# Kernel optimization log

Measured on AMD Instinct MI355X. Metric: run time of the kernel, lower is better.

The kernel has to match this reference:

```python
import jax, jax.numpy as jnp
import numpy as np

B, TX, TY, D, H, DK, DFF, L, V = 64, 200, 100, 512, 8, 64, 2048, 4, 30


def _ln(x, g, b, eps=1e-5):
    m = x.mean(-1, keepdims=True)
    v = x.var(-1, keepdims=True)  # biased, matches torch LayerNorm
    return (x - m) * jax.lax.rsqrt(v + eps) * g + b


def _mha(k_in, v_in, q_in, qkv, pw, pb, pad_mask, causal):
    # qkv: [3, H, DK, D] (torch Linear layout [out, in]); scale uses C = d_model
    scale = float(q_in.shape[-1]) ** 0.5
    Q = jnp.einsum('btd,hkd->bhtk', q_in, qkv[0])
    K = jnp.einsum('bsd,hkd->bhsk', k_in, qkv[1])
    Vv = jnp.einsum('bsd,hvd->bhsv', v_in, qkv[2])
    W = jnp.einsum('bhtk,bhsk->bhts', Q, K) / scale  # [B,H,T,S]
    if causal:
        tril = jnp.tril(jnp.ones((q_in.shape[1], k_in.shape[1]), bool))
        W = jnp.where(tril, W, -jnp.inf)
    if pad_mask is not None:
        W = jnp.where(pad_mask[:, None] == 1, -jnp.inf, W)
    A = jax.nn.softmax(W, axis=-1)
    out = jnp.einsum('bhts,bhsv->bhtv', A, Vv)
    b_, h_, t_, dv = out.shape
    out = out.transpose(0, 2, 1, 3).reshape(b_, t_, h_ * dv)  # concat heads
    return out @ pw.T + pb


def _attn_block(k, v, q, qkv, pw, pb, g, b, pad_mask, causal):
    kn, vn, qn = _ln(k, g, b), _ln(v, g, b), _ln(q, g, b)
    # NOTE: residual from the NORMED query, as in the original code
    return qn + _mha(kn, vn, qn, qkv, pw, pb, pad_mask, causal)


def _ff_block(x, w1, b1, w2, b2, g, b):
    h = jax.nn.relu(_ln(x, g, b) @ w1.T + b1)
    return x + h @ w2.T + b2


def _forward(x, y, enc_qkv, enc_proj_w, enc_proj_b, enc_ln1_g, enc_ln1_b,
             enc_ff_w1, enc_ff_b1, enc_ff_w2, enc_ff_b2, enc_ln2_g, enc_ln2_b,
             dec_sa_qkv, dec_sa_proj_w, dec_sa_proj_b, dec_ln1_g, dec_ln1_b,
             dec_ca_qkv, dec_ca_proj_w, dec_ca_proj_b, dec_ln2_g, dec_ln2_b,
             dec_ff_w1, dec_ff_b1, dec_ff_w2, dec_ff_b2, dec_ln3_g, dec_ln3_b,
             ll_w, ll_b, x_mask, y_mask):
    enc = x
    for i in range(L):
        enc = _attn_block(enc, enc, enc, enc_qkv[i], enc_proj_w[i], enc_proj_b[i],
                          enc_ln1_g[i], enc_ln1_b[i], x_mask, False)
        enc = _ff_block(enc, enc_ff_w1[i], enc_ff_b1[i], enc_ff_w2[i], enc_ff_b2[i],
                        enc_ln2_g[i], enc_ln2_b[i])
    dec = y
    for i in range(L):
        dec = _attn_block(dec, dec, dec, dec_sa_qkv[i], dec_sa_proj_w[i], dec_sa_proj_b[i],
                          dec_ln1_g[i], dec_ln1_b[i], y_mask, True)
        dec = _attn_block(enc, enc, dec, dec_ca_qkv[i], dec_ca_proj_w[i], dec_ca_proj_b[i],
                          dec_ln2_g[i], dec_ln2_b[i], None, False)
        dec = _ff_block(dec, dec_ff_w1[i], dec_ff_b1[i], dec_ff_w2[i], dec_ff_b2[i],
                        dec_ln3_g[i], dec_ln3_b[i])
    return dec @ ll_w.T + ll_b


def setup_inputs() -> dict:
    key = jax.random.key(0)
    ks = iter(jax.random.split(key, 64))

    def nrm(shape, s=0.02):
        return jax.random.normal(next(ks), shape, jnp.float32) * s

    return dict(
        x=nrm((B, TX, D), 1.0), y=nrm((B, TY, D), 1.0),
        x_mask=jnp.zeros((B, TX, TX), jnp.int32),
        y_mask=jnp.zeros((B, TY, TY), jnp.int32),
        enc_qkv=nrm((L, 3, H, DK, D)), enc_proj_w=nrm((L, D, D)), enc_proj_b=jnp.zeros((L, D)),
        enc_ln1_g=jnp.ones((L, D)), enc_ln1_b=jnp.zeros((L, D)),
        enc_ff_w1=nrm((L, DFF, D)), enc_ff_b1=jnp.zeros((L, DFF)),
        enc_ff_w2=nrm((L, D, DFF)), enc_ff_b2=jnp.zeros((L, D)),
        enc_ln2_g=jnp.ones((L, D)), enc_ln2_b=jnp.zeros((L, D)),
        dec_sa_qkv=nrm((L, 3, H, DK, D)), dec_sa_proj_w=nrm((L, D, D)), dec_sa_proj_b=jnp.zeros((L, D)),
        dec_ln1_g=jnp.ones((L, D)), dec_ln1_b=jnp.zeros((L, D)),
        dec_ca_qkv=nrm((L, 3, H, DK, D)), dec_ca_proj_w=nrm((L, D, D)), dec_ca_proj_b=jnp.zeros((L, D)),
        dec_ln2_g=jnp.ones((L, D)), dec_ln2_b=jnp.zeros((L, D)),
        dec_ff_w1=nrm((L, DFF, D)), dec_ff_b1=jnp.zeros((L, DFF)),
        dec_ff_w2=nrm((L, D, DFF)), dec_ff_b2=jnp.zeros((L, D)),
        dec_ln3_g=jnp.ones((L, D)), dec_ln3_b=jnp.zeros((L, D)),
        ll_w=nrm((V, D)), ll_b=jnp.zeros((V,)),
    )


def reference(x, y, x_mask, y_mask, enc_qkv, enc_proj_w, enc_proj_b, enc_ln1_g, enc_ln1_b,
              enc_ff_w1, enc_ff_b1, enc_ff_w2, enc_ff_b2, enc_ln2_g, enc_ln2_b,
              dec_sa_qkv, dec_sa_proj_w, dec_sa_proj_b, dec_ln1_g, dec_ln1_b,
              dec_ca_qkv, dec_ca_proj_w, dec_ca_proj_b, dec_ln2_g, dec_ln2_b,
              dec_ff_w1, dec_ff_b1, dec_ff_w2, dec_ff_b2, dec_ln3_g, dec_ln3_b,
              ll_w, ll_b):
    return _forward(x, y, enc_qkv, enc_proj_w, enc_proj_b, enc_ln1_g, enc_ln1_b,
                    enc_ff_w1, enc_ff_b1, enc_ff_w2, enc_ff_b2, enc_ln2_g, enc_ln2_b,
                    dec_sa_qkv, dec_sa_proj_w, dec_sa_proj_b, dec_ln1_g, dec_ln1_b,
                    dec_ca_qkv, dec_ca_proj_w, dec_ca_proj_b, dec_ln2_g, dec_ln2_b,
                    dec_ff_w1, dec_ff_b1, dec_ff_w2, dec_ff_b2, dec_ln3_g, dec_ln3_b,
                    ll_w, ll_b, x_mask, y_mask)
```

## Files before the change

### kernel.cpp

```cpp
#include <hip/hip_runtime.h>
#include <math.h>

#define B_SZ   64
#define TX_SZ  200
#define TY_SZ  100
#define D_MODEL 512
#define H_SZ   8
#define DK_SZ  64
#define DFF_SZ 2048
#define L_SZ   4
#define V_SZ   30

#define NEG_BIG -1.0e30f

#define PSTRF 204
#define ATT_LDSF (4 * 16 * PSTRF)

typedef unsigned short u16;
typedef __attribute__((ext_vector_type(8))) short short8;
typedef __attribute__((ext_vector_type(4))) short short4t;
typedef __attribute__((ext_vector_type(4))) float f32x4;
typedef __attribute__((ext_vector_type(4))) unsigned short u16x4;

__device__ __forceinline__ float b2f(u16 h) {
    union { unsigned int u; float f; } v; v.u = ((unsigned int)h) << 16; return v.f;
}
__device__ __forceinline__ u16 f2b(float f) {
    union { float f; unsigned int u; } v; v.f = f;
    unsigned int r = v.u + 0x7fffu + ((v.u >> 16) & 1u);
    return (u16)(r >> 16);
}

#define GLD16(gp, lp) __builtin_amdgcn_global_load_lds( \
    (const __attribute__((address_space(1))) unsigned int*)(gp), \
    (__attribute__((address_space(3))) unsigned int*)(lp), 16, 0, 0)

__global__ __launch_bounds__(256)
void castw_kernel(const float* __restrict__ in, u16* __restrict__ out, int n4) {
    int i = blockIdx.x * 256 + threadIdx.x;
    if (i < n4) {
        f32x4 v = ((const f32x4*)in)[i];
        u16x4 o;
        o.x = f2b(v.x); o.y = f2b(v.y); o.z = f2b(v.z); o.w = f2b(v.w);
        ((u16x4*)out)[i] = o;
    }
}

__global__ __launch_bounds__(256)
void maskpack_kernel(const int* __restrict__ mask, unsigned* __restrict__ bits,
                     int rows, int S, int wpr) {
    int row = blockIdx.x * 4 + (threadIdx.x >> 6);
    int lane = threadIdx.x & 63;
    if (row >= rows) return;
    const int* mr = mask + (size_t)row * S;
    unsigned* br = bits + (size_t)row * wpr;
    for (int s0 = 0; s0 < S; s0 += 64) {
        int s = s0 + lane;
        int v = (s < S) ? mr[s] : 0;
        unsigned long long bm = __ballot(v == 1);
        if (lane == 0) {
            br[s0 >> 5] = (unsigned)bm;
            if ((s0 >> 5) + 1 < wpr) br[(s0 >> 5) + 1] = (unsigned)(bm >> 32);
        }
    }
}

__global__ __launch_bounds__(256)
void vtrans_kernel(const u16* __restrict__ V, int ldv, u16* __restrict__ Vt,
                   int S, int spad) {
    __shared__ u16 t[16][72];
    const int bh = blockIdx.x;
    const int s0 = blockIdx.y * 16;
    const int h = bh & 7, b = bh >> 3;
    const int tid = threadIdx.x;
    {
        int sl = tid >> 4, c4 = (tid & 15) * 4;
        int s = s0 + sl;
        int ss = (s < S) ? s : S - 1;
        u16x4 v = *(const u16x4*)(V + (size_t)(b * S + ss) * ldv + h * 64 + c4);
        *(u16x4*)&t[sl][c4] = v;
    }
    __syncthreads();
    int d = tid >> 2, j0 = (tid & 3) * 4;
    if (s0 + j0 < spad) {
        u16x4 o;
        o.x = (s0 + j0 + 0 < S) ? t[j0 + 0][d] : (u16)0;
        o.y = (s0 + j0 + 1 < S) ? t[j0 + 1][d] : (u16)0;
        o.z = (s0 + j0 + 2 < S) ? t[j0 + 2][d] : (u16)0;
        o.w = (s0 + j0 + 3 < S) ? t[j0 + 3][d] : (u16)0;
        *(u16x4*)(Vt + ((size_t)bh * 64 + d) * spad + s0 + j0) = o;
    }
}

__global__ __launch_bounds__(256)
void ln_kernel(const float* __restrict__ in, const float* __restrict__ g,
               const float* __restrict__ b, float* outf, u16* outb, int rows) {
    int row = blockIdx.x * 4 + (threadIdx.x >> 6);
    int lane = threadIdx.x & 63;
    if (row >= rows) return;
    const f32x4* xr = (const f32x4*)(in + (size_t)row * D_MODEL);
    f32x4 v0 = xr[lane];
    f32x4 v1 = xr[lane + 64];
    float s  = v0.x + v0.y + v0.z + v0.w + v1.x + v1.y + v1.z + v1.w;
    float ss = v0.x*v0.x + v0.y*v0.y + v0.z*v0.z + v0.w*v0.w
             + v1.x*v1.x + v1.y*v1.y + v1.z*v1.z + v1.w*v1.w;
    #pragma unroll
    for (int off = 1; off < 64; off <<= 1) {
        s  += __shfl_xor(s, off, 64);
        ss += __shfl_xor(ss, off, 64);
    }
    float mean = s * (1.0f / D_MODEL);
    float var  = ss * (1.0f / D_MODEL) - mean * mean;
    float rstd = rsqrtf(var + 1e-5f);
    f32x4 g0 = ((const f32x4*)g)[lane],      g1 = ((const f32x4*)g)[lane + 64];
    f32x4 b0 = ((const f32x4*)b)[lane],      b1 = ((const f32x4*)b)[lane + 64];
    f32x4 o0, o1;
    o0.x = (v0.x - mean) * rstd * g0.x + b0.x;
    o0.y = (v0.y - mean) * rstd * g0.y + b0.y;
    o0.z = (v0.z - mean) * rstd * g0.z + b0.z;
    o0.w = (v0.w - mean) * rstd * g0.w + b0.w;
    o1.x = (v1.x - mean) * rstd * g1.x + b1.x;
    o1.y = (v1.y - mean) * rstd * g1.y + b1.y;
    o1.z = (v1.z - mean) * rstd * g1.z + b1.z;
    o1.w = (v1.w - mean) * rstd * g1.w + b1.w;
    if (outf) {
        f32x4* of = (f32x4*)(outf + (size_t)row * D_MODEL);
        of[lane] = o0; of[lane + 64] = o1;
    }
    if (outb) {
        u16x4* ob = (u16x4*)(outb + (size_t)row * D_MODEL);
        u16x4 p0, p1;
        p0.x = f2b(o0.x); p0.y = f2b(o0.y); p0.z = f2b(o0.z); p0.w = f2b(o0.w);
        p1.x = f2b(o1.x); p1.y = f2b(o1.y); p1.z = f2b(o1.z); p1.w = f2b(o1.w);
        ob[lane] = p0; ob[lane + 64] = p1;
    }
}

template<int BN>
__global__ __launch_bounds__(256)
void gemm_mfma_t(const u16* __restrict__ A, int lda,
                 const u16* __restrict__ W, int ldw,
                 float* outf, int ldcf, u16* outb, int ldcb,
                 const float* __restrict__ bias,
                 const float* __restrict__ resid, int ldr,
                 int relu, int K, int NP, int q8) {
    constexpr int NJ = BN / 32;
    __shared__ u16 Alds[3][128 * 32];
    __shared__ u16 Blds[3][BN * 32];
    const int tid  = threadIdx.x;
    const int wave = tid >> 6, lane = tid & 63;
    const int lr = lane & 15, lq = lane >> 4;
    const int wm = (wave >> 1) * 64, wn = (wave & 1) * (BN / 2);
    const int bid = blockIdx.x;
    const int sid = q8 ? ((bid & 7) * q8 + (bid >> 3)) : bid;
    const int m0 = (sid / NP) * 128, n0 = (sid % NP) * BN;
    const int grow = tid >> 2;
    const int gcol = (tid & 3) * 8;
    const int woff = wave * 512;

    f32x4 zero = {0.f, 0.f, 0.f, 0.f};
    f32x4 acc[4][NJ];
    #pragma unroll
    for (int i = 0; i < 4; ++i)
        #pragma unroll
        for (int j = 0; j < NJ; ++j) acc[i][j] = zero;

    const u16* Ag = A + (size_t)m0 * lda;
    const u16* Wg = W + (size_t)n0 * ldw;

    auto stage = [&](int buf, int t) {
        int k0 = t << 5;
        GLD16(Ag + (size_t)grow * lda + k0 + gcol,        &Alds[buf][woff]);
        GLD16(Ag + (size_t)(64 + grow) * lda + k0 + gcol, &Alds[buf][2048 + woff]);
        GLD16(Wg + (size_t)grow * ldw + k0 + gcol,        &Blds[buf][woff]);
        if (BN == 128)
            GLD16(Wg + (size_t)(64 + grow) * ldw + k0 + gcol, &Blds[buf][2048 + woff]);
    };

    const int nt = K >> 5;
    stage(0, 0);
    stage(1, 1);
    int cur = 0;
    for (int t = 0; t < nt; ++t) {
        if (t + 2 < nt) {
            int sb = cur + 2; if (sb >= 3) sb -= 3;
            stage(sb, t + 2);
            if constexpr (BN == 128)
                asm volatile("s_waitcnt vmcnt(8)" ::: "memory");
            else
                asm volatile("s_waitcnt vmcnt(6)" ::: "memory");
        } else if (t + 1 < nt) {
            if constexpr (BN == 128)
                asm volatile("s_waitcnt vmcnt(4)" ::: "memory");
            else
                asm volatile("s_waitcnt vmcnt(3)" ::: "memory");
        } else {
            asm volatile("s_waitcnt vmcnt(0)" ::: "memory");
        }
        __builtin_amdgcn_s_barrier();
        __builtin_amdgcn_sched_barrier(0);
        short8 af[4], bfr[NJ];
        #pragma unroll
        for (int i = 0; i < 4; ++i)
            af[i] = *(const short8*)&Alds[cur][(wm + i * 16 + lr) * 32 + lq * 8];
        #pragma unroll
        for (int j = 0; j < NJ; ++j)
            bfr[j] = *(const short8*)&Blds[cur][(wn + j * 16 + lr) * 32 + lq * 8];
        #pragma unroll
        for (int i = 0; i < 4; ++i)
            #pragma unroll
            for (int j = 0; j < NJ; ++j)
                acc[i][j] = __builtin_amdgcn_mfma_f32_16x16x32_bf16(af[i], bfr[j], acc[i][j], 0, 0, 0);
        __builtin_amdgcn_s_barrier();
        __builtin_amdgcn_sched_barrier(0);
        cur = (cur + 1 == 3) ? 0 : cur + 1;
    }

    #pragma unroll
    for (int i = 0; i < 4; ++i) {
        #pragma unroll
        for (int r = 0; r < 4; ++r) {
            int m = m0 + wm + i * 16 + lq * 4 + r;
            #pragma unroll
            for (int j = 0; j < NJ; ++j) {
                int n = n0 + wn + j * 16 + lr;
                float c = acc[i][j][r];
                if (bias)  c += bias[n];
                if (resid) c += resid[(size_t)m * ldr + n];
                if (relu)  c = fmaxf(c, 0.f);
                if (outf) outf[(size_t)m * ldcf + n] = c;
                if (outb) outb[(size_t)m * ldcb + n] = f2b(c);
            }
        }
    }
}

__global__ __launch_bounds__(256, 2)
void attn_kernel(u16* __restrict__ Q, int ldq, const u16* __restrict__ K, int ldk,
                 const u16* __restrict__ Vt, int spad,
                 const unsigned* __restrict__ mbits, int mwpr,
                 int T, int S, int causal, float rscale) {
    __shared__ float Pl[ATT_LDSF];
    const int bh = blockIdx.x, tile = blockIdx.y;
    const int h = bh & 7, b = bh >> 3;
    const int tid = threadIdx.x, wave = tid >> 6, lane = tid & 63;
    const int lm = lane & 15, quad = lane >> 4;
    const int t0 = tile * 64 + wave * 16;
    if (t0 >= T) return;

    const u16* Kg = K + (size_t)(b * S) * ldk + h * DK_SZ;
    const u16* Vg = Vt + (size_t)bh * 64 * spad;
    u16* Qg = Q + (size_t)(b * T) * ldq + h * DK_SZ;

    const int stiles = (S + 15) >> 4;
    int stmax = stiles;
    if (causal) { int c = (t0 >> 4) + 1; if (c < stmax) stmax = c; }
    const int Scap8 = (S + 7) & ~7;
    int Pcap = stmax * 16; if (Pcap > Scap8) Pcap = Scap8;

    float* Pw = Pl + wave * (16 * PSTRF);

    int qr = t0 + lm; if (qr >= T) qr = T - 1;
    const u16* qrow = Qg + (size_t)qr * ldq;
    short8 qa0 = *(const short8*)(qrow + quad * 8);
    short8 qa1 = *(const short8*)(qrow + 32 + quad * 8);

    unsigned mrow[4][7];
    if (mbits) {
        #pragma unroll
        for (int r = 0; r < 4; ++r) {
            int t = t0 + quad * 4 + r;
            int tc = (t < T) ? t : T - 1;
            const unsigned* mp = mbits + (size_t)(b * T + tc) * mwpr;
            #pragma unroll
            for (int w = 0; w < 7; ++w)
                if (w < mwpr) mrow[r][w] = mp[w];
        }
    }

    short8 kb[13][2];
    #pragma unroll
    for (int st = 0; st < 13; ++st) if (st < stmax) {
        int srow = st * 16 + lm; if (srow >= S) srow = S - 1;
        const u16* kp = Kg + (size_t)srow * ldk + quad * 8;
        kb[st][0] = *(const short8*)kp;
        kb[st][1] = *(const short8*)(kp + 32);
    }

    const short8 zero8 = {0, 0, 0, 0, 0, 0, 0, 0};
    const f32x4 zerof = {0.f, 0.f, 0.f, 0.f};

    float mx[4] = {NEG_BIG, NEG_BIG, NEG_BIG, NEG_BIG};
    #pragma unroll
    for (int st = 0; st < 13; ++st) if (st < stmax) {
        f32x4 c = zerof;
        c = __builtin_amdgcn_mfma_f32_16x16x32_bf16(qa0, kb[st][0], c, 0, 0, 0);
        c = __builtin_amdgcn_mfma_f32_16x16x32_bf16(qa1, kb[st][1], c, 0, 0, 0);
        int s = st * 16 + lm;
        #pragma unroll
        for (int r = 0; r < 4; ++r) {
            int t = t0 + quad * 4 + r;
            bool valid = (s < S) && (!causal || s <= t);
            if (valid && mbits)
                valid = ((mrow[r][st >> 1] >> (((st & 1) << 4) + lm)) & 1u) == 0;
            float f = valid ? c[r] * rscale : NEG_BIG;
            mx[r] = fmaxf(mx[r], f);
            if (s < PSTRF) Pw[(quad * 4 + r) * PSTRF + s] = f;
        }
    }
    #pragma unroll
    for (int r = 0; r < 4; ++r) {
        #pragma unroll
        for (int off = 1; off < 16; off <<= 1)
            mx[r] = fmaxf(mx[r], __shfl_xor(mx[r], off, 64));
    }

    short8 vbr[7][4];
    #pragma unroll
    for (int kt = 0; kt < 7; ++kt) if (kt * 32 < Pcap) {
        int nq = (Pcap - kt * 32) >> 3;
        #pragma unroll
        for (int dt = 0; dt < 4; ++dt)
            vbr[kt][dt] = (quad < nq)
                ? *(const short8*)(Vg + (size_t)(dt * 16 + lm) * spad + kt * 32 + quad * 8)
                : zero8;
    }

    float sum[4] = {0.f, 0.f, 0.f, 0.f};
    #pragma unroll
    for (int st = 0; st < 13; ++st) if (st < stmax) {
        int col = st * 16 + lm;
        if (col < PSTRF) {
            #pragma unroll
            for (int r = 0; r < 4; ++r) {
                int idx = (quad * 4 + r) * PSTRF + col;
                float p = __expf(Pw[idx] - mx[r]);
                sum[r] += p;
                Pw[idx] = p;
            }
        }
    }
    float rden[4];
    #pragma unroll
    for (int r = 0; r < 4; ++r) {
        #pragma unroll
        for (int off = 1; off < 16; off <<= 1)
            sum[r] += __shfl_xor(sum[r], off, 64);
        rden[r] = (sum[r] > 0.f) ? 1.0f / sum[r] : 0.f;
    }

    f32x4 ov[4] = {zerof, zerof, zerof, zerof};
    #pragma unroll
    for (int kt = 0; kt < 7; ++kt) if (kt * 32 < Pcap) {
        int k0 = kt * 32;
        int nq = (Pcap - k0) >> 3;
        short8 pa = zero8;
        if (quad < nq) {
            const float* prow = Pw + lm * PSTRF + k0 + quad * 8;
            f32x4 p0 = *(const f32x4*)prow;
            f32x4 p1 = *(const f32x4*)(prow + 4);
            pa[0] = (short)f2b(p0.x); pa[1] = (short)f2b(p0.y);
            pa[2] = (short)f2b(p0.z); pa[3] = (short)f2b(p0.w);
            pa[4] = (short)f2b(p1.x); pa[5] = (short)f2b(p1.y);
            pa[6] = (short)f2b(p1.z); pa[7] = (short)f2b(p1.w);
        }
        #pragma unroll
        for (int dt = 0; dt < 4; ++dt)
            ov[dt] = __builtin_amdgcn_mfma_f32_16x16x32_bf16(pa, vbr[kt][dt], ov[dt], 0, 0, 0);
    }

    #pragma unroll
    for (int r = 0; r < 4; ++r) {
        int t = t0 + quad * 4 + r;
        if (t < T) {
            u16* orow = Qg + (size_t)t * ldq;
            #pragma unroll
            for (int dt = 0; dt < 4; ++dt)
                orow[dt * 16 + lm] = f2b(ov[dt][r] * rden[r]);
        }
    }
}

__global__ __launch_bounds__(256)
void logits_kernel(const float* __restrict__ X, const float* __restrict__ Wl,
                   const float* __restrict__ bl, float* __restrict__ out, int rows) {
    int idx = blockIdx.x * 256 + threadIdx.x;
    if (idx >= rows * V_SZ) return;
    int row = idx / V_SZ, v = idx % V_SZ;
    const f32x4* xr = (const f32x4*)(X + (size_t)row * D_MODEL);
    const f32x4* wr = (const f32x4*)(Wl + (size_t)v * D_MODEL);
    float acc = bl[v];
    #pragma unroll 4
    for (int k = 0; k < D_MODEL / 4; ++k) {
        f32x4 a = xr[k], w = wr[k];
        acc += a.x * w.x + a.y * w.y + a.z * w.z + a.w * w.w;
    }
    out[idx] = acc;
}

extern "C" void kernel_launch(void* const* d_in, const int* in_sizes, int n_in,
                              void* d_out, int out_size, void* d_ws, size_t ws_size,
                              hipStream_t stream) {
    const float* x          = (const float*)d_in[0];
    const float* y          = (const float*)d_in[1];
    const int*   x_mask     = (const int*)d_in[2];
    const int*   y_mask     = (const int*)d_in[3];
    const float* enc_qkv    = (const float*)d_in[4];
    const float* enc_proj_w = (const float*)d_in[5];
    const float* enc_proj_b = (const float*)d_in[6];
    const float* enc_ln1_g  = (const float*)d_in[7];
    const float* enc_ln1_b  = (const float*)d_in[8];
    const float* enc_ff_w1  = (const float*)d_in[9];
    const float* enc_ff_b1  = (const float*)d_in[10];
    const float* enc_ff_w2  = (const float*)d_in[11];
    const float* enc_ff_b2  = (const float*)d_in[12];
    const float* enc_ln2_g  = (const float*)d_in[13];
    const float* enc_ln2_b  = (const float*)d_in[14];
    const float* dec_sa_qkv    = (const float*)d_in[15];
    const float* dec_sa_proj_w = (const float*)d_in[16];
    const float* dec_sa_proj_b = (const float*)d_in[17];
    const float* dec_ln1_g  = (const float*)d_in[18];
    const float* dec_ln1_b  = (const float*)d_in[19];
    const float* dec_ca_qkv    = (const float*)d_in[20];
    const float* dec_ca_proj_w = (const float*)d_in[21];
    const float* dec_ca_proj_b = (const float*)d_in[22];
    const float* dec_ln2_g  = (const float*)d_in[23];
    const float* dec_ln2_b  = (const float*)d_in[24];
    const float* dec_ff_w1  = (const float*)d_in[25];
    const float* dec_ff_b1  = (const float*)d_in[26];
    const float* dec_ff_w2  = (const float*)d_in[27];
    const float* dec_ff_b2  = (const float*)d_in[28];
    const float* dec_ln3_g  = (const float*)d_in[29];
    const float* dec_ln3_b  = (const float*)d_in[30];
    const float* ll_w       = (const float*)d_in[31];
    const float* ll_b       = (const float*)d_in[32];

    const int ME = B_SZ * TX_SZ;
    const int MD = B_SZ * TY_SZ;
    const float rscale = 1.0f / sqrtf((float)D_MODEL);
    const int XWPR = (TX_SZ + 31) / 32;
    const int YWPR = (TY_SZ + 31) / 32;
    const int WQKV = 3 * D_MODEL * D_MODEL;
    const int WDD  = D_MODEL * D_MODEL;
    const int WFF  = DFF_SZ * D_MODEL;

    char* base = (char*)d_ws;
    size_t off = 0;
    auto alloc = [&](size_t bytes) {
        void* p = base + off;
        off = (off + bytes + 63) & ~(size_t)63;
        return p;
    };
    float* A_enc = (float*)alloc((size_t)ME * D_MODEL * 4);
    float* A_dec = (float*)alloc((size_t)MD * D_MODEL * 4);
    float* N1f   = (float*)alloc((size_t)ME * D_MODEL * 4);
    u16*   N1b   = (u16*)  alloc((size_t)ME * D_MODEL * 2);
    u16*   NQb   = (u16*)  alloc((size_t)MD * D_MODEL * 2);
    u16*   BIG   = (u16*)  alloc((size_t)ME * DFF_SZ * 2);
    u16*   Vt    = (u16*)  alloc((size_t)B_SZ * H_SZ * 64 * 208 * 2);
    unsigned* XMb = (unsigned*)alloc((size_t)ME * XWPR * 4);
    unsigned* YMb = (unsigned*)alloc((size_t)MD * YWPR * 4);
    u16* Wall = (u16*)alloc(((size_t)4 * (2 * WQKV + 2 * WDD + 4 * WFF + WQKV + WDD)) * 2);
    u16* Wqkv_e   = Wall;
    u16* Wproj_e  = Wqkv_e   + (size_t)4 * WQKV;
    u16* Wff1_e   = Wproj_e  + (size_t)4 * WDD;
    u16* Wff2_e   = Wff1_e   + (size_t)4 * WFF;
    u16* Wqkv_sa  = Wff2_e   + (size_t)4 * WFF;
    u16* Wproj_sa = Wqkv_sa  + (size_t)4 * WQKV;
    u16* Wqkv_ca  = Wproj_sa + (size_t)4 * WDD;
    u16* Wproj_ca = Wqkv_ca  + (size_t)4 * WQKV;
    u16* Wff1_d   = Wproj_ca + (size_t)4 * WDD;
    u16* Wff2_d   = Wff1_d   + (size_t)4 * WFF;
    u16* QKVb = BIG;
    u16* Hb   = BIG;
    u16* KVb  = BIG;
    u16* Qca  = BIG + (size_t)ME * 1024;

    auto castw = [&](const float* in, u16* out, size_t n) {
        size_t n4 = n / 4;
        hipLaunchKernelGGL(castw_kernel, dim3((unsigned)((n4 + 255) / 256)), dim3(256), 0, stream,
                           in, out, (int)n4);
    };
    auto ln = [&](const float* in, const float* g, const float* b,
                  float* outf, u16* outb, int rows) {
        hipLaunchKernelGGL(ln_kernel, dim3(rows / 4), dim3(256), 0, stream, in, g, b, outf, outb, rows);
    };
    auto gemm = [&](const u16* A, int lda, const u16* W, int ldw, int M, int N, int K,
                    float* outf, int ldcf, u16* outb, int ldcb,
                    const float* bias, const float* resid, int ldr, int relu) {
        int blocks128 = (M / 128) * (N / 128);
        if (blocks128 < 512) {
            int NP = N / 64, nwg = (M / 128) * NP;
            int q8 = (nwg % 8 == 0) ? nwg / 8 : 0;
            hipLaunchKernelGGL((gemm_mfma_t<64>), dim3(nwg), dim3(256), 0, stream,
                               A, lda, W, ldw, outf, ldcf, outb, ldcb, bias, resid, ldr, relu,
                               K, NP, q8);
        } else {
            int NP = N / 128, nwg = (M / 128) * NP;
            int q8 = (nwg % 8 == 0) ? nwg / 8 : 0;
            hipLaunchKernelGGL((gemm_mfma_t<128>), dim3(nwg), dim3(256), 0, stream,
                               A, lda, W, ldw, outf, ldcf, outb, ldcb, bias, resid, ldr, relu,
                               K, NP, q8);
        }
    };
    auto vtrans = [&](const u16* V, int ldv, int S, int spad) {
        dim3 grid(B_SZ * H_SZ, (spad + 15) / 16);
        hipLaunchKernelGGL(vtrans_kernel, grid, dim3(256), 0, stream, V, ldv, Vt, S, spad);
    };
    auto attn = [&](u16* Q, int ldq, const u16* K, int ldk, int spad,
                    const unsigned* mbits, int mwpr, int T, int S, int causal) {
        dim3 grid(B_SZ * H_SZ, (T + 63) / 64);
        hipLaunchKernelGGL(attn_kernel, grid, dim3(256), 0, stream,
                           Q, ldq, K, ldk, Vt, spad, mbits, mwpr, T, S, causal, rscale);
    };

    hipLaunchKernelGGL(maskpack_kernel, dim3((ME + 3) / 4), dim3(256), 0, stream,
                       x_mask, XMb, ME, TX_SZ, XWPR);
    hipLaunchKernelGGL(maskpack_kernel, dim3((MD + 3) / 4), dim3(256), 0, stream,
                       y_mask, YMb, MD, TY_SZ, YWPR);
    castw(enc_qkv,        Wqkv_e,   (size_t)4 * WQKV);
    castw(enc_proj_w,     Wproj_e,  (size_t)4 * WDD);
    castw(enc_ff_w1,      Wff1_e,   (size_t)4 * WFF);
    castw(enc_ff_w2,      Wff2_e,   (size_t)4 * WFF);
    castw(dec_sa_qkv,     Wqkv_sa,  (size_t)4 * WQKV);
    castw(dec_sa_proj_w,  Wproj_sa, (size_t)4 * WDD);
    castw(dec_ca_qkv,     Wqkv_ca,  (size_t)4 * WQKV);
    castw(dec_ca_proj_w,  Wproj_ca, (size_t)4 * WDD);
    castw(dec_ff_w1,      Wff1_d,   (size_t)4 * WFF);
    castw(dec_ff_w2,      Wff2_d,   (size_t)4 * WFF);

    for (int l = 0; l < L_SZ; ++l) {
        const float* src = (l == 0) ? x : A_enc;
        ln(src, enc_ln1_g + l * D_MODEL, enc_ln1_b + l * D_MODEL, N1f, N1b, ME);
        gemm(N1b, 512, Wqkv_e + (size_t)l * WQKV, 512, ME, 1536, 512,
             nullptr, 0, QKVb, 1536, nullptr, nullptr, 0, 0);
        vtrans(QKVb + 1024, 1536, TX_SZ, 200);
        attn(QKVb, 1536, QKVb + 512, 1536, 200, XMb, XWPR, TX_SZ, TX_SZ, 0);
        gemm(QKVb, 1536, Wproj_e + (size_t)l * WDD, 512, ME, 512, 512,
             A_enc, 512, nullptr, 0, enc_proj_b + l * D_MODEL, N1f, 512, 0);
        ln(A_enc, enc_ln2_g + l * D_MODEL, enc_ln2_b + l * D_MODEL, nullptr, N1b, ME);
        gemm(N1b, 512, Wff1_e + (size_t)l * WFF, 512, ME, 2048, 512,
             nullptr, 0, Hb, 2048, enc_ff_b1 + l * DFF_SZ, nullptr, 0, 1);
        gemm(Hb, 2048, Wff2_e + (size_t)l * WFF, 2048, ME, 512, 2048,
             A_enc, 512, nullptr, 0, enc_ff_b2 + l * D_MODEL, A_enc, 512, 0);
    }

    for (int l = 0; l < L_SZ; ++l) {
        const float* src = (l == 0) ? y : A_dec;
        ln(src, dec_ln1_g + l * D_MODEL, dec_ln1_b + l * D_MODEL, N1f, N1b, MD);
        gemm(N1b, 512, Wqkv_sa + (size_t)l * WQKV, 512, MD, 1536, 512,
             nullptr, 0, QKVb, 1536, nullptr, nullptr, 0, 0);
        vtrans(QKVb + 1024, 1536, TY_SZ, 104);
        attn(QKVb, 1536, QKVb + 512, 1536, 104, YMb, YWPR, TY_SZ, TY_SZ, 1);
        gemm(QKVb, 1536, Wproj_sa + (size_t)l * WDD, 512, MD, 512, 512,
             A_dec, 512, nullptr, 0, dec_sa_proj_b + l * D_MODEL, N1f, 512, 0);
        ln(A_enc, dec_ln2_g + l * D_MODEL, dec_ln2_b + l * D_MODEL, nullptr, N1b, ME);
        ln(A_dec, dec_ln2_g + l * D_MODEL, dec_ln2_b + l * D_MODEL, N1f, NQb, MD);
        gemm(NQb, 512, Wqkv_ca + (size_t)l * WQKV, 512, MD, 512, 512,
             nullptr, 0, Qca, 512, nullptr, nullptr, 0, 0);
        gemm(N1b, 512, Wqkv_ca + (size_t)l * WQKV + WDD, 512, ME, 1024, 512,
             nullptr, 0, KVb, 1024, nullptr, nullptr, 0, 0);
        vtrans(KVb + 512, 1024, TX_SZ, 200);
        attn(Qca, 512, KVb, 1024, 200, nullptr, XWPR, TY_SZ, TX_SZ, 0);
        gemm(Qca, 512, Wproj_ca + (size_t)l * WDD, 512, MD, 512, 512,
             A_dec, 512, nullptr, 0, dec_ca_proj_b + l * D_MODEL, N1f, 512, 0);
        ln(A_dec, dec_ln3_g + l * D_MODEL, dec_ln3_b + l * D_MODEL, nullptr, N1b, MD);
        gemm(N1b, 512, Wff1_d + (size_t)l * WFF, 512, MD, 2048, 512,
             nullptr, 0, Hb, 2048, dec_ff_b1 + l * DFF_SZ, nullptr, 0, 1);
        gemm(Hb, 2048, Wff2_d + (size_t)l * WFF, 2048, MD, 512, 2048,
             A_dec, 512, nullptr, 0, dec_ff_b2 + l * D_MODEL, A_dec, 512, 0);
    }

    {
        int total = MD * V_SZ;
        hipLaunchKernelGGL(logits_kernel, dim3((total + 255) / 256), dim3(256), 0, stream,
                           A_dec, ll_w, ll_b, (float*)d_out, MD);
    }
    (void)in_sizes; (void)n_in; (void)out_size; (void)ws_size;
}
```

Before: 2.674 ms.

## Add 256x256-tile 512-thread bf16 MFMA GEMM for large-grid GEMMs

Adds a GEMM kernel with 256x256 output tiles, 8 waves per block and double-buffered 64-wide K stages in LDS. The host dispatcher routes a GEMM to it when M and N are multiples of 256 and the grid would have at least 250 blocks, which covers the large encoder projections such as QKV and FF1. Larger tiles raise operand reuse and cut global and LDS traffic per MFMA. In exchange it needs about 128 KB of LDS per block and 128 accumulator registers per lane, which limits occupancy and may cause register pressure or spills. It also uses a two-stage pipeline where the existing kernel uses three.

```diff
diff --git a/kernel.cpp b/kernel.cpp
--- a/kernel.cpp
+++ b/kernel.cpp
@@ -224,6 +224,97 @@
             #pragma unroll
             for (int j = 0; j < NJ; ++j) {
                 int n = n0 + wn + j * 16 + lr;
+                float c = acc[i][j][r];
+                if (bias)  c += bias[n];
+                if (resid) c += resid[(size_t)m * ldr + n];
+                if (relu)  c = fmaxf(c, 0.f);
+                if (outf) outf[(size_t)m * ldcf + n] = c;
+                if (outb) outb[(size_t)m * ldcb + n] = f2b(c);
+            }
+        }
+    }
+}
+
+__global__ __launch_bounds__(512, 2)
+void gemm_mfma_256(const u16* __restrict__ A, int lda,
+                   const u16* __restrict__ W, int ldw,
+                   float* outf, int ldcf, u16* outb, int ldcb,
+                   const float* __restrict__ bias,
+                   const float* __restrict__ resid, int ldr,
+                   int relu, int K, int NP, int q8) {
+    __shared__ u16 Al[2][256 * 64];
+    __shared__ u16 Bl[2][256 * 64];
+    const int tid = threadIdx.x;
+    const int lane = tid & 63, wave = tid >> 6;
+    const int lr = lane & 15, lq = lane >> 4;
+    const int wr = wave >> 2, wc = wave & 3;
+    const int bid = blockIdx.x;
+    const int sid = q8 ? ((bid & 7) * q8 + (bid >> 3)) : bid;
+    const int m0 = (sid / NP) * 256, n0 = (sid % NP) * 256;
+    const int grow = tid >> 3;
+    const int gcol = (tid & 7) * 8;
+
+    f32x4 zero = {0.f, 0.f, 0.f, 0.f};
+    f32x4 acc[8][4];
+    #pragma unroll
+    for (int i = 0; i < 8; ++i)
+        #pragma unroll
+        for (int j = 0; j < 4; ++j) acc[i][j] = zero;
+
+    const u16* Ag = A + (size_t)m0 * lda;
+    const u16* Wg = W + (size_t)n0 * ldw;
+
+    auto stage = [&](int buf, int t) {
+        int k0 = t << 6;
+        #pragma unroll
+        for (int i = 0; i < 4; ++i) {
+            GLD16(Ag + (size_t)(i * 64 + grow) * lda + k0 + gcol,
+                  &Al[buf][i * 4096 + tid * 8]);
+            GLD16(Wg + (size_t)(i * 64 + grow) * ldw + k0 + gcol,
+                  &Bl[buf][i * 4096 + tid * 8]);
+        }
+    };
+
+    const int nt = K >> 6;
+    stage(0, 0);
+    int cur = 0;
+    for (int t = 0; t < nt; ++t) {
+        if (t + 1 < nt) {
+            stage(cur ^ 1, t + 1);
+            asm volatile("s_waitcnt vmcnt(8)" ::: "memory");
+        } else {
+            asm volatile("s_waitcnt vmcnt(0)" ::: "memory");
+        }
+        __builtin_amdgcn_s_barrier();
+        __builtin_amdgcn_sched_barrier(0);
+        #pragma unroll
+        for (int kh = 0; kh < 2; ++kh) {
+            short8 af[8], bfv[4];
+            #pragma unroll
+            for (int i = 0; i < 8; ++i)
+                af[i] = *(const short8*)&Al[cur][(wr * 128 + i * 16 + lr) * 64 + kh * 32 + lq * 8];
+            #pragma unroll
+            for (int j = 0; j < 4; ++j)
+                bfv[j] = *(const short8*)&Bl[cur][(wc * 64 + j * 16 + lr) * 64 + kh * 32 + lq * 8];
+            #pragma unroll
+            for (int i = 0; i < 8; ++i)
+                #pragma unroll
+                for (int j = 0; j < 4; ++j)
+                    acc[i][j] = __builtin_amdgcn_mfma_f32_16x16x32_bf16(af[i], bfv[j], acc[i][j], 0, 0, 0);
+        }
+        __builtin_amdgcn_s_barrier();
+        __builtin_amdgcn_sched_barrier(0);
+        cur ^= 1;
+    }
+
+    #pragma unroll
+    for (int i = 0; i < 8; ++i) {
+        #pragma unroll
+        for (int r = 0; r < 4; ++r) {
+            int m = m0 + wr * 128 + i * 16 + lq * 4 + r;
+            #pragma unroll
+            for (int j = 0; j < 4; ++j) {
+                int n = n0 + wc * 64 + j * 16 + lr;
                 float c = acc[i][j][r];
                 if (bias)  c += bias[n];
                 if (resid) c += resid[(size_t)m * ldr + n];
@@ -488,6 +579,16 @@
     auto gemm = [&](const u16* A, int lda, const u16* W, int ldw, int M, int N, int K,
                     float* outf, int ldcf, u16* outb, int ldcb,
                     const float* bias, const float* resid, int ldr, int relu) {
+        int blocks256 = ((M % 256) == 0 && (N % 256) == 0 && (K & 63) == 0)
+                        ? (M / 256) * (N / 256) : 0;
+        if (blocks256 >= 250) {
+            int NP = N / 256, nwg = blocks256;
+            int q8 = (nwg % 8 == 0) ? nwg / 8 : 0;
+            hipLaunchKernelGGL(gemm_mfma_256, dim3(nwg), dim3(512), 0, stream,
+                               A, lda, W, ldw, outf, ldcf, outb, ldcb, bias, resid, ldr, relu,
+                               K, NP, q8);
+            return;
+        }
         int blocks128 = (M / 128) * (N / 128);
         if (blocks128 < 512) {
             int NP = N / 64, nwg = (M / 128) * NP;
```

After: 2.814 ms. 1.05x slower.
